# Kernel optimization log

Measured on AMD Instinct MI355X. Metric: run time of the kernel, lower is better.

## Reference

```python
import jax, jax.numpy as jnp
import numpy as np

NUM_GROUPS = 64  # number of distinct gt object ids (fill_max of gt_inds_*)
EPS = 1e-05
LOSS_WEIGHT = 1.0


def dice_coefficient(x, target):
    # x, target: [N, H, W] -> per-instance dice loss [N]
    n = x.shape[0]
    x = x.reshape(n, -1)
    t = target.reshape(n, -1)
    intersection = jnp.sum(x * t, axis=1)
    union = jnp.sum(x * x, axis=1) + jnp.sum(t * t, axis=1) + EPS
    return 1.0 - 2.0 * intersection / union


def setup_inputs() -> dict:
    key = jax.random.key(0)
    ks = jax.random.split(key, 6)
    preds_T = jax.random.normal(ks[0], (256, 256, 256), dtype=jnp.float32)
    preds_S = jax.random.normal(ks[1], (128, 256, 256), dtype=jnp.float32)
    gt_T = jax.random.uniform(ks[2], (256, 256, 256), dtype=jnp.float32)
    gt_S = jax.random.uniform(ks[3], (128, 256, 256), dtype=jnp.float32)
    gt_inds_T = jax.random.randint(ks[4], (256,), 0, NUM_GROUPS)
    gt_inds_S = jax.random.randint(ks[5], (128,), 0, NUM_GROUPS)
    return {
        "preds_T": preds_T,
        "preds_S": preds_S,
        "im_ind": 0,
        "gt_T": gt_T,
        "gt_S": gt_S,
        "iter": 1,
        "gt_inds_T": gt_inds_T,
        "gt_inds_S": gt_inds_S,
    }


def reference(preds_T, preds_S, im_ind, gt_T, gt_S, iter, gt_inds_T, gt_inds_S):
    # 1) per-teacher-instance dice vs teacher gt masks
    iou_loss = dice_coefficient(preds_T, gt_T)  # [N_T]

    # 2) 'nms': per gt group, pick the teacher instance with min loss
    #    (single fused segment-argmin instead of a python loop over unique ids)
    group_mask = gt_inds_T[:, None] == jnp.arange(NUM_GROUPS)[None, :]  # [N_T, G]
    masked_loss = jnp.where(group_mask, iou_loss[:, None], jnp.inf)
    best_idx = jnp.argmin(masked_loss, axis=0)  # [G] best teacher instance per group
    present = jnp.any(group_mask, axis=0)       # [G] group has >=1 teacher instance

    # 3) 'match': pair each student instance with the nms'd teacher mask of its gt id;
    #    instances whose gt id has no teacher instance contribute nothing
    matched_T = preds_T[best_idx[gt_inds_S]]  # [N_S, H, W]
    valid = present[gt_inds_S]                # [N_S]

    # 4) dice between matched teacher/student masks, masked sum
    per_pair = dice_coefficient(preds_S, matched_T)  # [N_S]
    return LOSS_WEIGHT * jnp.sum(jnp.where(valid, per_pair, 0.0))
```

## Files before the change

### kernel.cpp

```cpp
#include <hip/hip_runtime.h>
#include <math.h>

#define NPIX 65536
#define NGROUPS 64
#define DICE_EPS 1e-5f
#define SPLIT_T 8
#define SPLIT_S 16
#define MAX_NT 256

__global__ __launch_bounds__(256) void teacher_partial(
    const float* __restrict__ preds_T, const float* __restrict__ gt_T,
    float* __restrict__ acc_T) {
  const int i = blockIdx.x / SPLIT_T;
  const int c = blockIdx.x % SPLIT_T;
  const size_t base = (size_t)i * NPIX + (size_t)c * (NPIX / SPLIT_T);
  const float4* __restrict__ x = (const float4*)(preds_T + base);
  const float4* __restrict__ t = (const float4*)(gt_T + base);

  float inter = 0.f, xx = 0.f, tt = 0.f;
  const int n4 = NPIX / SPLIT_T / 4;
  for (int k = threadIdx.x; k < n4; k += 256) {
    float4 a = x[k];
    float4 b = t[k];
    inter += a.x * b.x + a.y * b.y + a.z * b.z + a.w * b.w;
    xx    += a.x * a.x + a.y * a.y + a.z * a.z + a.w * a.w;
    tt    += b.x * b.x + b.y * b.y + b.z * b.z + b.w * b.w;
  }
  for (int off = 32; off > 0; off >>= 1) {
    inter += __shfl_down(inter, off);
    xx    += __shfl_down(xx, off);
    tt    += __shfl_down(tt, off);
  }
  __shared__ float s[3][4];
  const int wave = threadIdx.x >> 6, lane = threadIdx.x & 63;
  if (lane == 0) { s[0][wave] = inter; s[1][wave] = xx; s[2][wave] = tt; }
  __syncthreads();
  if (threadIdx.x == 0) {
    float I = 0.f, X = 0.f, T = 0.f;
    for (int w = 0; w < 4; ++w) { I += s[0][w]; X += s[1][w]; T += s[2][w]; }
    atomicAdd(&acc_T[i * 3 + 0], I);
    atomicAdd(&acc_T[i * 3 + 1], X);
    atomicAdd(&acc_T[i * 3 + 2], T);
  }
}

__global__ __launch_bounds__(256) void finalize_nms(
    const float* __restrict__ acc_T, const int* __restrict__ gt_inds_T, int nT,
    float* __restrict__ xx_T, int* __restrict__ best_idx,
    int* __restrict__ present) {
  __shared__ float iou[MAX_NT];
  const int i = threadIdx.x;
  if (i < nT) {
    float I = acc_T[i * 3 + 0], X = acc_T[i * 3 + 1], T = acc_T[i * 3 + 2];
    iou[i] = 1.f - 2.f * I / (X + T + DICE_EPS);
    xx_T[i] = X;
  }
  __syncthreads();
  if (i < NGROUPS) {
    float bv = INFINITY;
    int bi = 0, pres = 0;
    for (int k = 0; k < nT; ++k) {
      if (gt_inds_T[k] == i) {
        pres = 1;
        float v = iou[k];
        if (v < bv) { bv = v; bi = k; }
      }
    }
    best_idx[i] = bi;
    present[i] = pres;
  }
}

__global__ __launch_bounds__(256) void student_partial(
    const float* __restrict__ preds_S, const float* __restrict__ preds_T,
    const int* __restrict__ gt_inds_S, const int* __restrict__ best_idx,
    const int* __restrict__ present, float* __restrict__ acc_S) {
  const int s = blockIdx.x / SPLIT_S;
  const int c = blockIdx.x % SPLIT_S;
  const int g = gt_inds_S[s];
  if (!present[g]) return;
  const int j = best_idx[g];

  const size_t off_s = (size_t)s * NPIX + (size_t)c * (NPIX / SPLIT_S);
  const size_t off_t = (size_t)j * NPIX + (size_t)c * (NPIX / SPLIT_S);
  const float4* __restrict__ x = (const float4*)(preds_S + off_s);
  const float4* __restrict__ t = (const float4*)(preds_T + off_t);

  float inter = 0.f, xx = 0.f;
  const int n4 = NPIX / SPLIT_S / 4;
  for (int k = threadIdx.x; k < n4; k += 256) {
    float4 a = x[k];
    float4 b = t[k];
    inter += a.x * b.x + a.y * b.y + a.z * b.z + a.w * b.w;
    xx    += a.x * a.x + a.y * a.y + a.z * a.z + a.w * a.w;
  }
  for (int off = 32; off > 0; off >>= 1) {
    inter += __shfl_down(inter, off);
    xx    += __shfl_down(xx, off);
  }
  __shared__ float s2[2][4];
  const int wave = threadIdx.x >> 6, lane = threadIdx.x & 63;
  if (lane == 0) { s2[0][wave] = inter; s2[1][wave] = xx; }
  __syncthreads();
  if (threadIdx.x == 0) {
    float I = 0.f, X = 0.f;
    for (int w = 0; w < 4; ++w) { I += s2[0][w]; X += s2[1][w]; }
    atomicAdd(&acc_S[s * 2 + 0], I);
    atomicAdd(&acc_S[s * 2 + 1], X);
  }
}

__global__ __launch_bounds__(128) void student_final(
    const float* __restrict__ acc_S, const float* __restrict__ xx_T,
    const int* __restrict__ gt_inds_S, const int* __restrict__ best_idx,
    const int* __restrict__ present, float* __restrict__ out, int nS) {
  float v = 0.f;
  const int s = threadIdx.x;
  if (s < nS) {
    const int g = gt_inds_S[s];
    if (present[g]) {
      const int j = best_idx[g];
      float I = acc_S[s * 2 + 0], X = acc_S[s * 2 + 1];
      v = 1.f - 2.f * I / (X + xx_T[j] + DICE_EPS);
    }
  }
  for (int off = 32; off > 0; off >>= 1) v += __shfl_down(v, off);
  __shared__ float p[2];
  if ((threadIdx.x & 63) == 0) p[threadIdx.x >> 6] = v;
  __syncthreads();
  if (threadIdx.x == 0) *out = p[0] + p[1];
}

extern "C" void kernel_launch(void* const* d_in, const int* in_sizes, int n_in,
                              void* d_out, int out_size, void* d_ws, size_t ws_size,
                              hipStream_t stream) {
  const float* preds_T = (const float*)d_in[0];
  const float* preds_S = (const float*)d_in[1];
  const float* gt_T    = (const float*)d_in[3];
  const int* gt_inds_T = (const int*)d_in[6];
  const int* gt_inds_S = (const int*)d_in[7];
  float* out = (float*)d_out;

  const int nT = in_sizes[6];
  const int nS = in_sizes[7];

  float* acc_T   = (float*)d_ws;
  float* acc_S   = acc_T + (size_t)nT * 3;
  float* xx_T    = acc_S + (size_t)nS * 2;
  int*   best_idx = (int*)(xx_T + nT);
  int*   present  = best_idx + NGROUPS;

  hipMemsetAsync(d_ws, 0, ((size_t)nT * 3 + (size_t)nS * 2) * sizeof(float),
                 stream);

  teacher_partial<<<nT * SPLIT_T, 256, 0, stream>>>(preds_T, gt_T, acc_T);
  finalize_nms<<<1, 256, 0, stream>>>(acc_T, gt_inds_T, nT, xx_T, best_idx,
                                      present);
  student_partial<<<nS * SPLIT_S, 256, 0, stream>>>(preds_S, preds_T,
                                                    gt_inds_S, best_idx,
                                                    present, acc_S);
  student_final<<<1, 128, 0, stream>>>(acc_S, xx_T, gt_inds_S, best_idx,
                                       present, out, nS);
}
```

Baseline: 72.36 us.

## Move student self-norm into teacher pass and unroll streaming loads

```diff
diff --git a/kernel.cpp b/kernel.cpp
--- a/kernel.cpp
+++ b/kernel.cpp
@@ -8,39 +8,78 @@
 #define SPLIT_S 16
 #define MAX_NT 256
 
-__global__ __launch_bounds__(256) void teacher_partial(
+__global__ __launch_bounds__(256) void stream_partials(
     const float* __restrict__ preds_T, const float* __restrict__ gt_T,
-    float* __restrict__ acc_T) {
-  const int i = blockIdx.x / SPLIT_T;
-  const int c = blockIdx.x % SPLIT_T;
-  const size_t base = (size_t)i * NPIX + (size_t)c * (NPIX / SPLIT_T);
-  const float4* __restrict__ x = (const float4*)(preds_T + base);
-  const float4* __restrict__ t = (const float4*)(gt_T + base);
-
-  float inter = 0.f, xx = 0.f, tt = 0.f;
-  const int n4 = NPIX / SPLIT_T / 4;
-  for (int k = threadIdx.x; k < n4; k += 256) {
-    float4 a = x[k];
-    float4 b = t[k];
-    inter += a.x * b.x + a.y * b.y + a.z * b.z + a.w * b.w;
-    xx    += a.x * a.x + a.y * a.y + a.z * a.z + a.w * a.w;
-    tt    += b.x * b.x + b.y * b.y + b.z * b.z + b.w * b.w;
-  }
-  for (int off = 32; off > 0; off >>= 1) {
-    inter += __shfl_down(inter, off);
-    xx    += __shfl_down(xx, off);
-    tt    += __shfl_down(tt, off);
-  }
-  __shared__ float s[3][4];
-  const int wave = threadIdx.x >> 6, lane = threadIdx.x & 63;
-  if (lane == 0) { s[0][wave] = inter; s[1][wave] = xx; s[2][wave] = tt; }
-  __syncthreads();
-  if (threadIdx.x == 0) {
-    float I = 0.f, X = 0.f, T = 0.f;
-    for (int w = 0; w < 4; ++w) { I += s[0][w]; X += s[1][w]; T += s[2][w]; }
-    atomicAdd(&acc_T[i * 3 + 0], I);
-    atomicAdd(&acc_T[i * 3 + 1], X);
-    atomicAdd(&acc_T[i * 3 + 2], T);
+    const float* __restrict__ preds_S, int nT,
+    float* __restrict__ acc_T, float* __restrict__ acc_S) {
+  const int tid = threadIdx.x;
+  const int tBlocks = nT * SPLIT_T;
+  __shared__ float sm[3][4];
+  const int wave = tid >> 6, lane = tid & 63;
+
+  if ((int)blockIdx.x < tBlocks) {
+    const int i = blockIdx.x / SPLIT_T;
+    const int c = blockIdx.x % SPLIT_T;
+    const size_t base = (size_t)i * NPIX + (size_t)c * (NPIX / SPLIT_T);
+    const float4* __restrict__ x = (const float4*)(preds_T + base);
+    const float4* __restrict__ t = (const float4*)(gt_T + base);
+
+    float inter = 0.f, xx = 0.f, tt = 0.f;
+    float4 a[4], b[4];
+#pragma unroll
+    for (int h = 0; h < 2; ++h) {
+      const int o = h * 1024 + tid;
+#pragma unroll
+      for (int u = 0; u < 4; ++u) a[u] = x[o + u * 256];
+#pragma unroll
+      for (int u = 0; u < 4; ++u) b[u] = t[o + u * 256];
+#pragma unroll
+      for (int u = 0; u < 4; ++u) {
+        inter += a[u].x * b[u].x + a[u].y * b[u].y + a[u].z * b[u].z + a[u].w * b[u].w;
+        xx    += a[u].x * a[u].x + a[u].y * a[u].y + a[u].z * a[u].z + a[u].w * a[u].w;
+        tt    += b[u].x * b[u].x + b[u].y * b[u].y + b[u].z * b[u].z + b[u].w * b[u].w;
+      }
+    }
+    for (int off = 32; off > 0; off >>= 1) {
+      inter += __shfl_down(inter, off);
+      xx    += __shfl_down(xx, off);
+      tt    += __shfl_down(tt, off);
+    }
+    if (lane == 0) { sm[0][wave] = inter; sm[1][wave] = xx; sm[2][wave] = tt; }
+    __syncthreads();
+    if (tid == 0) {
+      float I = 0.f, X = 0.f, T = 0.f;
+      for (int w = 0; w < 4; ++w) { I += sm[0][w]; X += sm[1][w]; T += sm[2][w]; }
+      atomicAdd(&acc_T[i * 3 + 0], I);
+      atomicAdd(&acc_T[i * 3 + 1], X);
+      atomicAdd(&acc_T[i * 3 + 2], T);
+    }
+  } else {
+    const int sb = blockIdx.x - tBlocks;
+    const int s = sb / SPLIT_T;
+    const int c = sb % SPLIT_T;
+    const size_t base = (size_t)s * NPIX + (size_t)c * (NPIX / SPLIT_T);
+    const float4* __restrict__ x = (const float4*)(preds_S + base);
+
+    float xx = 0.f;
+    float4 a[4];
+#pragma unroll
+    for (int h = 0; h < 2; ++h) {
+      const int o = h * 1024 + tid;
+#pragma unroll
+      for (int u = 0; u < 4; ++u) a[u] = x[o + u * 256];
+#pragma unroll
+      for (int u = 0; u < 4; ++u)
+        xx += a[u].x * a[u].x + a[u].y * a[u].y + a[u].z * a[u].z + a[u].w * a[u].w;
+    }
+    for (int off = 32; off > 0; off >>= 1) xx += __shfl_down(xx, off);
+    if (lane == 0) sm[0][wave] = xx;
+    __syncthreads();
+    if (tid == 0) {
+      float X = 0.f;
+      for (int w = 0; w < 4; ++w) X += sm[0][w];
+      atomicAdd(&acc_S[s * 2 + 1], X);
+    }
   }
 }
 
@@ -49,10 +88,12 @@
     float* __restrict__ xx_T, int* __restrict__ best_idx,
     int* __restrict__ present) {
   __shared__ float iou[MAX_NT];
+  __shared__ int ginds[MAX_NT];
   const int i = threadIdx.x;
   if (i < nT) {
     float I = acc_T[i * 3 + 0], X = acc_T[i * 3 + 1], T = acc_T[i * 3 + 2];
     iou[i] = 1.f - 2.f * I / (X + T + DICE_EPS);
+    ginds[i] = gt_inds_T[i];
     xx_T[i] = X;
   }
   __syncthreads();
@@ -60,7 +101,7 @@
     float bv = INFINITY;
     int bi = 0, pres = 0;
     for (int k = 0; k < nT; ++k) {
-      if (gt_inds_T[k] == i) {
+      if (ginds[k] == i) {
         pres = 1;
         float v = iou[k];
         if (v < bv) { bv = v; bi = k; }
@@ -71,7 +112,7 @@
   }
 }
 
-__global__ __launch_bounds__(256) void student_partial(
+__global__ __launch_bounds__(256) void cross_partial(
     const float* __restrict__ preds_S, const float* __restrict__ preds_T,
     const int* __restrict__ gt_inds_S, const int* __restrict__ best_idx,
     const int* __restrict__ present, float* __restrict__ acc_S) {
@@ -86,27 +127,24 @@
   const float4* __restrict__ x = (const float4*)(preds_S + off_s);
   const float4* __restrict__ t = (const float4*)(preds_T + off_t);
 
-  float inter = 0.f, xx = 0.f;
-  const int n4 = NPIX / SPLIT_S / 4;
-  for (int k = threadIdx.x; k < n4; k += 256) {
-    float4 a = x[k];
-    float4 b = t[k];
-    inter += a.x * b.x + a.y * b.y + a.z * b.z + a.w * b.w;
-    xx    += a.x * a.x + a.y * a.y + a.z * a.z + a.w * a.w;
-  }
-  for (int off = 32; off > 0; off >>= 1) {
-    inter += __shfl_down(inter, off);
-    xx    += __shfl_down(xx, off);
-  }
-  __shared__ float s2[2][4];
-  const int wave = threadIdx.x >> 6, lane = threadIdx.x & 63;
-  if (lane == 0) { s2[0][wave] = inter; s2[1][wave] = xx; }
+  float inter = 0.f;
+  float4 a[4], b[4];
+  const int tid = threadIdx.x;
+#pragma unroll
+  for (int u = 0; u < 4; ++u) a[u] = x[tid + u * 256];
+#pragma unroll
+  for (int u = 0; u < 4; ++u) b[u] = t[tid + u * 256];
+#pragma unroll
+  for (int u = 0; u < 4; ++u)
+    inter += a[u].x * b[u].x + a[u].y * b[u].y + a[u].z * b[u].z + a[u].w * b[u].w;
+
+  for (int off = 32; off > 0; off >>= 1) inter += __shfl_down(inter, off);
+  __shared__ float sm[4];
+  if ((tid & 63) == 0) sm[tid >> 6] = inter;
   __syncthreads();
-  if (threadIdx.x == 0) {
-    float I = 0.f, X = 0.f;
-    for (int w = 0; w < 4; ++w) { I += s2[0][w]; X += s2[1][w]; }
+  if (tid == 0) {
+    float I = sm[0] + sm[1] + sm[2] + sm[3];
     atomicAdd(&acc_S[s * 2 + 0], I);
-    atomicAdd(&acc_S[s * 2 + 1], X);
   }
 }
 
@@ -144,21 +182,21 @@
   const int nT = in_sizes[6];
   const int nS = in_sizes[7];
 
-  float* acc_T   = (float*)d_ws;
-  float* acc_S   = acc_T + (size_t)nT * 3;
-  float* xx_T    = acc_S + (size_t)nS * 2;
+  float* acc_T    = (float*)d_ws;
+  float* acc_S    = acc_T + (size_t)nT * 3;
+  float* xx_T     = acc_S + (size_t)nS * 2;
   int*   best_idx = (int*)(xx_T + nT);
   int*   present  = best_idx + NGROUPS;
 
   hipMemsetAsync(d_ws, 0, ((size_t)nT * 3 + (size_t)nS * 2) * sizeof(float),
                  stream);
 
-  teacher_partial<<<nT * SPLIT_T, 256, 0, stream>>>(preds_T, gt_T, acc_T);
+  stream_partials<<<nT * SPLIT_T + nS * SPLIT_T, 256, 0, stream>>>(
+      preds_T, gt_T, preds_S, nT, acc_T, acc_S);
   finalize_nms<<<1, 256, 0, stream>>>(acc_T, gt_inds_T, nT, xx_T, best_idx,
                                       present);
-  student_partial<<<nS * SPLIT_S, 256, 0, stream>>>(preds_S, preds_T,
-                                                    gt_inds_S, best_idx,
-                                                    present, acc_S);
+  cross_partial<<<nS * SPLIT_S, 256, 0, stream>>>(preds_S, preds_T, gt_inds_S,
+                                                  best_idx, present, acc_S);
   student_final<<<1, 128, 0, stream>>>(acc_S, xx_T, gt_inds_S, best_idx,
                                        present, out, nS);
 }
```

After: 71.01 us. About the same (-1.9%).
